# Kernel tuning notes

Hardware: AMD Instinct MI355X
Metric: run time of the kernel (lower is better)

The kernel has to match this reference:

```python
import jax, jax.numpy as jnp
import numpy as np

N = 100_000   # nodes
E = 1_600_000 # edges
G = 64        # graphs in batch
IN_FEAT, H = 8, 16
NUM_CLASSES = 4


def _glorot(key, fi, fo):
    lim = float(np.sqrt(6.0 / (fi + fo)))
    return jax.random.uniform(key, (fi, fo), jnp.float32, -lim, lim)


def setup_inputs() -> dict:
    key = jax.random.key(0)
    ks = jax.random.split(key, 12)
    inp = {
        "x": jax.random.normal(ks[0], (N, IN_FEAT), jnp.float32),
        "edge_src": jax.random.randint(ks[1], (E,), 0, N, dtype=jnp.int32),
        "edge_dst": jax.random.randint(ks[2], (E,), 0, N, dtype=jnp.int32),
        "batch": jnp.sort(jax.random.randint(ks[3], (N,), 0, G, dtype=jnp.int32)),
    }
    dims = [(IN_FEAT, H), (H, 2 * H), (2 * H, 4 * H), (4 * H, 8 * H)]
    for i, (fi, fo) in enumerate(dims, 1):
        inp[f"W{i}"] = _glorot(ks[3 + i], fi, fo)
        inp[f"b{i}"] = jnp.zeros((fo,), jnp.float32)
    # PReLU slopes (torch default init 0.25, single parameter)
    inp["a1"] = jnp.float32(0.25)
    inp["a2"] = jnp.float32(0.25)
    inp["a3"] = jnp.float32(0.25)
    inp["Wlin"] = _glorot(ks[8], 8 * H, NUM_CLASSES)
    inp["blin"] = jnp.zeros((NUM_CLASSES,), jnp.float32)
    return inp


def _prelu(x, a):
    return jnp.where(x >= 0, x, a * x)


def reference(x, edge_src, edge_dst, batch,
              W1, b1, W2, b2, W3, b3, W4, b4,
              a1, a2, a3, Wlin, blin):
    # GCNConv: add self-loops, symmetric normalization D^-1/2 A_hat D^-1/2
    loops = jnp.arange(N, dtype=edge_src.dtype)
    src = jnp.concatenate([edge_src, loops])  # [E+N]
    dst = jnp.concatenate([edge_dst, loops])
    deg = jax.ops.segment_sum(jnp.ones_like(src, jnp.float32), dst, num_segments=N)
    dinv = jax.lax.rsqrt(jnp.maximum(deg, 1.0))
    norm = dinv[src] * dinv[dst]  # [E+N]

    def gcn(h, W, b):
        h = h @ W                                   # [N, Fout]
        msg = h[src] * norm[:, None]                # gather + edge scale
        return jax.ops.segment_sum(msg, dst, num_segments=N) + b

    h = _prelu(gcn(x, W1, b1), a1)
    h = _prelu(gcn(h, W2, b2), a2)
    h = _prelu(gcn(h, W3, b3), a3)
    h = gcn(h, W4, b4)

    # global mean pool over graphs
    sums = jax.ops.segment_sum(h, batch, num_segments=G)          # [G, 8H]
    cnts = jax.ops.segment_sum(jnp.ones((N,), jnp.float32), batch, num_segments=G)
    pooled = sums / jnp.maximum(cnts, 1.0)[:, None]
    # dropout(p=0.25) is identity at inference
    return pooled @ Wlin + blin                                    # [G, 4]
```

## Files before the change

### kernel.cpp

```cpp
#include <hip/hip_runtime.h>
#include <hip/hip_fp16.h>

#define NN 100000
#define NE 1600000
#define NG 64

#define BSHIFT 7
#define BUCKW (1 << BSHIFT)
#define NBUCK ((NN + BUCKW - 1) >> BSHIFT)
#define BCAP 2560
#define BIN_CHUNK 4096

union H8 { float4 f4; __half2 h2[4]; };
union H4 { float2 f2; __half2 h2[2]; };
__device__ __forceinline__ void h8_to_f(const H8& h, float* f) {
    float2 a = __half22float2(h.h2[0]);
    float2 b = __half22float2(h.h2[1]);
    float2 c = __half22float2(h.h2[2]);
    float2 d = __half22float2(h.h2[3]);
    f[0]=a.x; f[1]=a.y; f[2]=b.x; f[3]=b.y; f[4]=c.x; f[5]=c.y; f[6]=d.x; f[7]=d.y;
}
__device__ __forceinline__ H8 f_to_h8(const float* f) {
    H8 h;
    h.h2[0] = __floats2half2_rn(f[0], f[1]);
    h.h2[1] = __floats2half2_rn(f[2], f[3]);
    h.h2[2] = __floats2half2_rn(f[4], f[5]);
    h.h2[3] = __floats2half2_rn(f[6], f[7]);
    return h;
}
__device__ __forceinline__ float prelu_f(float x, float s) {
    return fmaxf(x, 0.f) + s * fminf(x, 0.f);
}

__global__ __launch_bounds__(256) void bin_kernel(const int* __restrict__ src,
                                                  const int* __restrict__ dst,
                                                  int* __restrict__ bcnt,
                                                  unsigned* __restrict__ binned, int E) {
    __shared__ int h[NBUCK];
    __shared__ int cur[NBUCK];
    for (int i = threadIdx.x; i < NBUCK; i += 256) h[i] = 0;
    __syncthreads();
    int base = blockIdx.x * BIN_CHUNK;
    int end = base + BIN_CHUNK; if (end > E) end = E;
    for (int e = base + threadIdx.x; e < end; e += 256)
        atomicAdd(&h[dst[e] >> BSHIFT], 1);
    __syncthreads();
    for (int i = threadIdx.x; i < NBUCK; i += 256) {
        int c = h[i];
        cur[i] = c ? (i * BCAP + atomicAdd(&bcnt[i], c)) : 0;
    }
    __syncthreads();
    for (int e = base + threadIdx.x; e < end; e += 256) {
        unsigned s = (unsigned)src[e], d = (unsigned)dst[e];
        int pos = atomicAdd(&cur[d >> BSHIFT], 1);
        binned[pos] = (s << BSHIFT) | (d & (BUCKW - 1));
    }
}

__global__ __launch_bounds__(256) void build_csr_kernel(
    const unsigned* __restrict__ binned, const int* __restrict__ bucket_cnt,
    const float4* __restrict__ x4, float4* __restrict__ xs,
    int* __restrict__ deg, float* __restrict__ dinv,
    int* __restrict__ roff, int* __restrict__ csr_src, int n) {
    __shared__ int ldeg[BUCKW];
    __shared__ int lscan[2][BUCKW];
    __shared__ int lcur[BUCKW];
    int b = blockIdx.x;
    int tid = threadIdx.x;
    for (int i = tid; i < BUCKW; i += 256) ldeg[i] = 0;
    __syncthreads();
    int start = b * BCAP, cnt = bucket_cnt[b];
    for (int k = tid; k < cnt; k += 256)
        atomicAdd(&ldeg[binned[start + k] & (BUCKW - 1)], 1);
    __syncthreads();
    if (tid < BUCKW) lscan[0][tid] = ldeg[tid];
    __syncthreads();
    int cur = 0;
    for (int off = 1; off < BUCKW; off <<= 1) {
        int x = 0;
        if (tid < BUCKW) {
            x = lscan[cur][tid];
            if (tid >= off) x += lscan[cur][tid - off];
        }
        __syncthreads();
        if (tid < BUCKW) lscan[cur ^ 1][tid] = x;
        __syncthreads();
        cur ^= 1;
    }
    int v0 = b << BSHIFT;
    if (tid < BUCKW) {
        int v = v0 + tid;
        if (v < n) {
            int dg = ldeg[tid];
            deg[v] = dg;
            float dv = rsqrtf((float)dg + 1.0f);
            dinv[v] = dv;
            float4 h0 = x4[(size_t)v * 2 + 0];
            float4 h1 = x4[(size_t)v * 2 + 1];
            h0.x *= dv; h0.y *= dv; h0.z *= dv; h0.w *= dv;
            h1.x *= dv; h1.y *= dv; h1.z *= dv; h1.w *= dv;
            xs[(size_t)v * 2 + 0] = h0;
            xs[(size_t)v * 2 + 1] = h1;
            int r = start + lscan[cur][tid] - dg;
            roff[v] = r;
            lcur[tid] = r;
        }
    }
    __syncthreads();
    for (int k = tid; k < cnt; k += 256) {
        unsigned e = binned[start + k];
        int pos = atomicAdd(&lcur[e & (BUCKW - 1)], 1);
        csr_src[pos] = (int)(e >> BSHIFT);
    }
}

__global__ __launch_bounds__(256) void makeM_kernel(
    const float* __restrict__ W4, const float* __restrict__ b4,
    const float* __restrict__ Wlin, const float* __restrict__ blin,
    float* __restrict__ M, float* __restrict__ bb) {
    int t = threadIdx.x;
    int k = t >> 2, c = t & 3;
    float m = 0.f;
    for (int j = 0; j < 128; ++j) m += W4[k * 128 + j] * Wlin[j * 4 + c];
    M[k * 4 + c] = m;
    if (t < 4) {
        float v = blin[t];
        for (int j = 0; j < 128; ++j) v += b4[j] * Wlin[j * 4 + t];
        bb[t] = v;
    }
}

__global__ __launch_bounds__(256) void aggmm1_kernel(
    const float4* __restrict__ xs, const int* __restrict__ row_off,
    const int* __restrict__ deg, const float* __restrict__ dinv,
    const int* __restrict__ csr_src, const float* __restrict__ W1,
    const float* __restrict__ b1, const float* __restrict__ a1,
    float2* __restrict__ Aout2, int n) {
    __shared__ float Wl[8 * 16];
    for (int i = threadIdx.x; i < 8 * 16; i += 256) Wl[i] = W1[i];
    __syncthreads();
    int idx = blockIdx.x * 256 + threadIdx.x;
    if (idx >= n * 4) return;
    int v = idx >> 2;
    int c = idx & 1;
    int h = (idx >> 1) & 1;
    float4 acc = (h == 0) ? xs[(size_t)v * 2 + c] : make_float4(0.f, 0.f, 0.f, 0.f);
    int start = row_off[v], cnt = deg[v];
    int mid = cnt >> 1;
    int beg = h ? mid : 0;
    int myend = h ? cnt : mid;
    const int* __restrict__ row = csr_src + start;
    int j = beg;
    for (; j + 4 <= myend; j += 4) {
        int s0 = row[j], s1 = row[j + 1], s2 = row[j + 2], s3 = row[j + 3];
        float4 a0 = xs[(size_t)s0 * 2 + c];
        float4 a1v = xs[(size_t)s1 * 2 + c];
        float4 a2 = xs[(size_t)s2 * 2 + c];
        float4 a3 = xs[(size_t)s3 * 2 + c];
        acc.x += (a0.x + a1v.x) + (a2.x + a3.x);
        acc.y += (a0.y + a1v.y) + (a2.y + a3.y);
        acc.z += (a0.z + a1v.z) + (a2.z + a3.z);
        acc.w += (a0.w + a1v.w) + (a2.w + a3.w);
    }
    for (; j < myend; ++j) {
        int s = row[j];
        float4 a = xs[(size_t)s * 2 + c];
        acc.x += a.x; acc.y += a.y; acc.z += a.z; acc.w += a.w;
    }
    acc.x += __shfl_xor(acc.x, 2, 64);
    acc.y += __shfl_xor(acc.y, 2, 64);
    acc.z += __shfl_xor(acc.z, 2, 64);
    acc.w += __shfl_xor(acc.w, 2, 64);
    float dvv = dinv[v];
    float t[4] = { acc.x * dvv, acc.y * dvv, acc.z * dvv, acc.w * dvv };
    float po[4];
#pragma unroll
    for (int k = 0; k < 4; ++k) po[k] = __shfl_xor(t[k], 1, 64);
    int ow = (h * 2 + c) * 4;
    int e0 = c * 4, e1 = 4 - e0;
    float accm[4];
#pragma unroll
    for (int q = 0; q < 4; ++q) accm[q] = b1[ow + q];
#pragma unroll
    for (int k = 0; k < 4; ++k) {
        float r1 = t[k], r2 = po[k];
        const float* w1 = &Wl[(e0 + k) * 16 + ow];
        const float* w2 = &Wl[(e1 + k) * 16 + ow];
#pragma unroll
        for (int q = 0; q < 4; ++q) accm[q] += r1 * w1[q] + r2 * w2[q];
    }
    float s = *a1;
    float o[4];
#pragma unroll
    for (int q = 0; q < 4; ++q) o[q] = prelu_f(accm[q], s) * dvv;
    H4 ho;
    ho.h2[0] = __floats2half2_rn(o[0], o[1]);
    ho.h2[1] = __floats2half2_rn(o[2], o[3]);
    Aout2[(size_t)v * 4 + (h * 2 + c)] = ho.f2;
}

__global__ __launch_bounds__(256) void aggmm2_kernel(
    const float4* __restrict__ hs, const int* __restrict__ row_off,
    const int* __restrict__ deg, const float* __restrict__ dinv,
    const int* __restrict__ csr_src, const float* __restrict__ W2,
    const float* __restrict__ b2, const float* __restrict__ a2,
    float4* __restrict__ Aout, int n) {
    __shared__ float Wl[16 * 32];
    for (int i = threadIdx.x; i < 16 * 32; i += 256) Wl[i] = W2[i];
    __syncthreads();
    int idx = blockIdx.x * 256 + threadIdx.x;
    if (idx >= n * 4) return;
    int v = idx >> 2;
    int c = idx & 1;
    int h = (idx >> 1) & 1;
    float a[8];
    if (h == 0) { H8 t; t.f4 = hs[(size_t)v * 2 + c]; h8_to_f(t, a); }
    else {
#pragma unroll
        for (int k = 0; k < 8; ++k) a[k] = 0.f;
    }
    int start = row_off[v], cnt = deg[v];
    int mid = cnt >> 1;
    int beg = h ? mid : 0;
    int myend = h ? cnt : mid;
    const int* __restrict__ row = csr_src + start;
    int j = beg;
    for (; j + 4 <= myend; j += 4) {
        H8 hh[4];
#pragma unroll
        for (int q = 0; q < 4; ++q) hh[q].f4 = hs[(size_t)row[j + q] * 2 + c];
#pragma unroll
        for (int q = 0; q < 4; ++q) {
            float f[8]; h8_to_f(hh[q], f);
#pragma unroll
            for (int k = 0; k < 8; ++k) a[k] += f[k];
        }
    }
    for (; j < myend; ++j) {
        H8 t; t.f4 = hs[(size_t)row[j] * 2 + c];
        float f[8]; h8_to_f(t, f);
#pragma unroll
        for (int k = 0; k < 8; ++k) a[k] += f[k];
    }
#pragma unroll
    for (int k = 0; k < 8; ++k) a[k] += __shfl_xor(a[k], 2, 64);
    float dvv = dinv[v];
#pragma unroll
    for (int k = 0; k < 8; ++k) a[k] *= dvv;
    float pa[8];
#pragma unroll
    for (int k = 0; k < 8; ++k) pa[k] = __shfl_xor(a[k], 1, 64);
    int ow = (h * 2 + c) * 8;
    int e0 = c * 8, e1 = 8 - e0;
    float accm[8];
#pragma unroll
    for (int q = 0; q < 8; ++q) accm[q] = b2[ow + q];
#pragma unroll
    for (int k = 0; k < 8; ++k) {
        float r1 = a[k], r2 = pa[k];
        const float* w1 = &Wl[(e0 + k) * 32 + ow];
        const float* w2 = &Wl[(e1 + k) * 32 + ow];
#pragma unroll
        for (int q = 0; q < 8; ++q) accm[q] += r1 * w1[q] + r2 * w2[q];
    }
    float s = *a2;
    float o[8];
#pragma unroll
    for (int q = 0; q < 8; ++q) o[q] = prelu_f(accm[q], s) * dvv;
    H8 ho = f_to_h8(o);
    Aout[(size_t)v * 4 + (h * 2 + c)] = ho.f4;
}

__global__ __launch_bounds__(256) void aggmm3_kernel(
    const float4* __restrict__ hs, const int* __restrict__ row_off,
    const int* __restrict__ deg, const float* __restrict__ dinv,
    const int* __restrict__ csr_src, const float* __restrict__ W3,
    const float* __restrict__ b3, const float* __restrict__ a3,
    const float* __restrict__ M, float4* __restrict__ z, int n) {
    __shared__ float Wl[32 * 64];
    __shared__ float Ml[64 * 4];
    for (int i = threadIdx.x; i < 32 * 64; i += 256) Wl[i] = W3[i];
    for (int i = threadIdx.x; i < 64 * 4; i += 256) Ml[i] = M[i];
    __syncthreads();
    int idx = blockIdx.x * 256 + threadIdx.x;
    if (idx >= n * 8) return;
    int v = idx >> 3;
    int c = idx & 3;
    int h = (idx >> 2) & 1;
    float a[8];
    if (h == 0) { H8 t; t.f4 = hs[(size_t)v * 4 + c]; h8_to_f(t, a); }
    else {
#pragma unroll
        for (int k = 0; k < 8; ++k) a[k] = 0.f;
    }
    int start = row_off[v], cnt = deg[v];
    int mid = cnt >> 1;
    int beg = h ? mid : 0;
    int myend = h ? cnt : mid;
    const int* __restrict__ row = csr_src + start;
    int j = beg;
    for (; j + 4 <= myend; j += 4) {
        H8 hh[4];
#pragma unroll
        for (int q = 0; q < 4; ++q) hh[q].f4 = hs[(size_t)row[j + q] * 4 + c];
#pragma unroll
        for (int q = 0; q < 4; ++q) {
            float f[8]; h8_to_f(hh[q], f);
#pragma unroll
            for (int k = 0; k < 8; ++k) a[k] += f[k];
        }
    }
    for (; j < myend; ++j) {
        H8 t; t.f4 = hs[(size_t)row[j] * 4 + c];
        float f[8]; h8_to_f(t, f);
#pragma unroll
        for (int k = 0; k < 8; ++k) a[k] += f[k];
    }
#pragma unroll
    for (int k = 0; k < 8; ++k) a[k] += __shfl_xor(a[k], 4, 64);
    float dvv = dinv[v];
#pragma unroll
    for (int k = 0; k < 8; ++k) a[k] *= dvv;
    int ow = (h * 4 + c) * 8;
    float accm[8];
#pragma unroll
    for (int q = 0; q < 8; ++q) accm[q] = b3[ow + q];
#pragma unroll
    for (int m = 0; m < 4; ++m) {
        float cur[8];
        if (m == 0) {
#pragma unroll
            for (int k = 0; k < 8; ++k) cur[k] = a[k];
        } else {
#pragma unroll
            for (int k = 0; k < 8; ++k) cur[k] = __shfl_xor(a[k], m, 64);
        }
        int eb = (c ^ m) * 8;
#pragma unroll
        for (int k = 0; k < 8; ++k) {
            float rk = cur[k];
            const float* wp = &Wl[(eb + k) * 64 + ow];
#pragma unroll
            for (int q = 0; q < 8; ++q) accm[q] += rk * wp[q];
        }
    }
    float s = *a3;
    float px = 0.f, py = 0.f, pz = 0.f, pw = 0.f;
#pragma unroll
    for (int q = 0; q < 8; ++q) {
        float o = prelu_f(accm[q], s) * dvv;
        const float* mp = &Ml[(ow + q) * 4];
        px += o * mp[0]; py += o * mp[1]; pz += o * mp[2]; pw += o * mp[3];
    }
#pragma unroll
    for (int mask = 1; mask <= 4; mask <<= 1) {
        px += __shfl_xor(px, mask, 64);
        py += __shfl_xor(py, mask, 64);
        pz += __shfl_xor(pz, mask, 64);
        pw += __shfl_xor(pw, mask, 64);
    }
    if ((idx & 7) == 0) z[v] = make_float4(px, py, pz, pw);
}

__global__ __launch_bounds__(256) void aggpool4_kernel(
    const float4* __restrict__ z, const int* __restrict__ row_off,
    const int* __restrict__ deg, const float* __restrict__ dinv,
    const int* __restrict__ csr_src, const int* __restrict__ batch,
    float* __restrict__ sums, float* __restrict__ cnt, int n) {
    __shared__ float lacc[NG * 4];
    __shared__ float lcnt[NG];
    int tid = threadIdx.x;
    if (tid < NG * 4) lacc[tid] = 0.f;
    if (tid < NG) lcnt[tid] = 0.f;
    __syncthreads();
    int idx = blockIdx.x * 256 + tid;
    bool valid = (idx < n * 2);
    int v = idx >> 1;
    int h = idx & 1;
    float cx = 0.f, cy = 0.f, cz = 0.f, cw = 0.f, rc = 0.f;
    int g = -1;
    if (valid) {
        float4 acc = (h == 0) ? z[v] : make_float4(0.f, 0.f, 0.f, 0.f);
        int start = row_off[v], dcnt = deg[v];
        int mid = dcnt >> 1;
        int beg = h ? mid : 0;
        int myend = h ? dcnt : mid;
        const int* __restrict__ row = csr_src + start;
        int j = beg;
        for (; j + 4 <= myend; j += 4) {
            float4 a0 = z[row[j]];
            float4 a1 = z[row[j + 1]];
            float4 a2 = z[row[j + 2]];
            float4 a3 = z[row[j + 3]];
            acc.x += (a0.x + a1.x) + (a2.x + a3.x);
            acc.y += (a0.y + a1.y) + (a2.y + a3.y);
            acc.z += (a0.z + a1.z) + (a2.z + a3.z);
            acc.w += (a0.w + a1.w) + (a2.w + a3.w);
        }
        for (; j < myend; ++j) {
            float4 a = z[row[j]];
            acc.x += a.x; acc.y += a.y; acc.z += a.z; acc.w += a.w;
        }
        cx = acc.x; cy = acc.y; cz = acc.z; cw = acc.w;
        g = batch[v];
    }
    cx += __shfl_xor(cx, 1, 64);
    cy += __shfl_xor(cy, 1, 64);
    cz += __shfl_xor(cz, 1, 64);
    cw += __shfl_xor(cw, 1, 64);
    if (valid) {
        float dv = dinv[v];
        cx *= dv; cy *= dv; cz *= dv; cw *= dv;
    }
    if (!valid || h == 1) { cx = cy = cz = cw = 0.f; rc = 0.f; }
    else rc = 1.f;
    int g0 = __shfl(g, 0, 64);
    if (__all(g == g0 || !valid)) {
#pragma unroll
        for (int mask = 32; mask >= 1; mask >>= 1) {
            cx += __shfl_xor(cx, mask, 64);
            cy += __shfl_xor(cy, mask, 64);
            cz += __shfl_xor(cz, mask, 64);
            cw += __shfl_xor(cw, mask, 64);
            rc += __shfl_xor(rc, mask, 64);
        }
        if ((tid & 63) == 0 && g0 >= 0) {
            float* lp = &lacc[g0 * 4];
            atomicAdd(lp + 0, cx); atomicAdd(lp + 1, cy);
            atomicAdd(lp + 2, cz); atomicAdd(lp + 3, cw);
            atomicAdd(&lcnt[g0], rc);
        }
    } else if (valid && h == 0) {
        float* lp = &lacc[g * 4];
        atomicAdd(lp + 0, cx); atomicAdd(lp + 1, cy);
        atomicAdd(lp + 2, cz); atomicAdd(lp + 3, cw);
        atomicAdd(&lcnt[g], 1.f);
    }
    __syncthreads();
    if (tid < NG * 4) {
        float val = lacc[tid];
        if (val != 0.f) atomicAdd(&sums[tid], val);
    }
    if (tid < NG) {
        float val = lcnt[tid];
        if (val != 0.f) atomicAdd(&cnt[tid], val);
    }
}

__global__ void head_kernel(const float* __restrict__ sums, const float* __restrict__ cnt,
                            const float* __restrict__ bb, float* __restrict__ out) {
    int t = threadIdx.x;
    int g = t >> 2, c = t & 3;
    out[t] = sums[t] / fmaxf(cnt[g], 1.f) + bb[c];
}

extern "C" void kernel_launch(void* const* d_in, const int* in_sizes, int n_in,
                              void* d_out, int out_size, void* d_ws, size_t ws_size,
                              hipStream_t stream) {
    const float* x    = (const float*)d_in[0];
    const int* esrc   = (const int*)d_in[1];
    const int* edst   = (const int*)d_in[2];
    const int* batch  = (const int*)d_in[3];
    const float* W1 = (const float*)d_in[4],  *b1 = (const float*)d_in[5];
    const float* W2 = (const float*)d_in[6],  *b2 = (const float*)d_in[7];
    const float* W3 = (const float*)d_in[8],  *b3 = (const float*)d_in[9];
    const float* W4 = (const float*)d_in[10], *b4 = (const float*)d_in[11];
    const float* a1 = (const float*)d_in[12];
    const float* a2 = (const float*)d_in[13];
    const float* a3 = (const float*)d_in[14];
    const float* Wlin = (const float*)d_in[15], *blin = (const float*)d_in[16];
    float* out = (float*)d_out;

    const int N = NN, E = NE;
    const int NBIN = (E + BIN_CHUNK - 1) / BIN_CHUNK;

    char* w = (char*)d_ws;
    size_t off = 0;
    auto alloc = [&](size_t bytes) { size_t r = off; off += (bytes + 255) & ~(size_t)255; return r; };
    size_t o_bcnt = alloc((size_t)NBUCK * 4);
    size_t o_pool = alloc((size_t)NG * 4 * 4);
    size_t o_cnt  = alloc((size_t)NG * 4);
    size_t zero_bytes = off;
    size_t o_deg  = alloc((size_t)N * 4);
    size_t o_dinv = alloc((size_t)N * 4);
    size_t o_roff = alloc((size_t)N * 4);
    size_t o_xs   = alloc((size_t)N * 8 * 4);
    size_t o_csrc = alloc((size_t)NBUCK * BCAP * 4);
    size_t o_bin  = alloc((size_t)NBUCK * BCAP * 4);
    size_t o_A1   = alloc((size_t)N * 16 * 2);
    size_t o_A2   = alloc((size_t)N * 32 * 2);
    size_t o_z    = alloc((size_t)N * 4 * 4);
    size_t o_M    = alloc((size_t)64 * 4 * 4);
    size_t o_bb   = alloc((size_t)4 * 4);
    (void)ws_size;
    int*      bcnt   = (int*)(w + o_bcnt);
    float*    pool   = (float*)(w + o_pool);
    float*    cnt    = (float*)(w + o_cnt);
    int*      deg    = (int*)(w + o_deg);
    float*    dinv   = (float*)(w + o_dinv);
    int*      roff   = (int*)(w + o_roff);
    float4*   xs     = (float4*)(w + o_xs);
    int*      csrc   = (int*)(w + o_csrc);
    unsigned* binned = (unsigned*)(w + o_bin);
    float2*   A1_2   = (float2*)(w + o_A1);
    float4*   A1     = (float4*)(w + o_A1);
    float4*   A2     = (float4*)(w + o_A2);
    float4*   z      = (float4*)(w + o_z);
    float*    M      = (float*)(w + o_M);
    float*    bb     = (float*)(w + o_bb);

    hipMemsetAsync(w, 0, zero_bytes, stream);

    makeM_kernel<<<1, 256, 0, stream>>>(W4, b4, Wlin, blin, M, bb);

    bin_kernel<<<NBIN, 256, 0, stream>>>(esrc, edst, bcnt, binned, E);
    build_csr_kernel<<<NBUCK, 256, 0, stream>>>(binned, bcnt, (const float4*)x, xs,
                                                deg, dinv, roff, csrc, N);

    aggmm1_kernel<<<(N * 4 + 255) / 256, 256, 0, stream>>>(
        xs, roff, deg, dinv, csrc, W1, b1, a1, A1_2, N);

    aggmm2_kernel<<<(N * 4 + 255) / 256, 256, 0, stream>>>(
        A1, roff, deg, dinv, csrc, W2, b2, a2, A2, N);

    aggmm3_kernel<<<(N * 8 + 255) / 256, 256, 0, stream>>>(
        A2, roff, deg, dinv, csrc, W3, b3, a3, M, z, N);

    aggpool4_kernel<<<(N * 2 + 255) / 256, 256, 0, stream>>>(
        z, roff, deg, dinv, csrc, batch, pool, cnt, N);
    head_kernel<<<1, 256, 0, stream>>>(pool, cnt, bb, out);
}
```

Baseline: 224.6 us.

## Use coarser 1024-node buckets for CSR build with register-cached edge binning

The buckets used to bin edges by destination grow from 128 to 1024 nodes, giving 98 buckets instead of 782. The CSR build kernel now runs one 1024-thread block per bucket. The binning kernel loads each edge's src and dst into registers once and reuses them for both the histogram and scatter passes, with smaller chunks per block. This cuts global atomics on bucket counters and repeated edge reads. In exchange, far fewer blocks run the CSR build, each does a longer 10-step scan, and the bucket capacity bound (18432) must hold for the random inputs.

```diff
diff --git a/kernel.cpp b/kernel.cpp
--- a/kernel.cpp
+++ b/kernel.cpp
@@ -5,11 +5,11 @@
 #define NE 1600000
 #define NG 64
 
-#define BSHIFT 7
-#define BUCKW (1 << BSHIFT)
-#define NBUCK ((NN + BUCKW - 1) >> BSHIFT)
-#define BCAP 2560
-#define BIN_CHUNK 4096
+#define BSHIFT_C 10
+#define BUCKW_C (1 << BSHIFT_C)
+#define NBUCK_C ((NN + BUCKW_C - 1) >> BSHIFT_C)
+#define BCAP_C 18432
+#define BIN_CHUNK 2048
 
 union H8 { float4 f4; __half2 h2[4]; };
 union H4 { float2 f2; __half2 h2[2]; };
@@ -36,81 +36,89 @@
                                                   const int* __restrict__ dst,
                                                   int* __restrict__ bcnt,
                                                   unsigned* __restrict__ binned, int E) {
-    __shared__ int h[NBUCK];
-    __shared__ int cur[NBUCK];
-    for (int i = threadIdx.x; i < NBUCK; i += 256) h[i] = 0;
+    __shared__ int h[NBUCK_C];
+    __shared__ int cur[NBUCK_C];
+    int tid = threadIdx.x;
+    for (int i = tid; i < NBUCK_C; i += 256) h[i] = 0;
     __syncthreads();
     int base = blockIdx.x * BIN_CHUNK;
     int end = base + BIN_CHUNK; if (end > E) end = E;
-    for (int e = base + threadIdx.x; e < end; e += 256)
-        atomicAdd(&h[dst[e] >> BSHIFT], 1);
-    __syncthreads();
-    for (int i = threadIdx.x; i < NBUCK; i += 256) {
+    int ms[8], md[8];
+#pragma unroll
+    for (int k = 0; k < 8; ++k) {
+        int e = base + k * 256 + tid;
+        if (e < end) { ms[k] = src[e]; md[k] = dst[e]; }
+    }
+#pragma unroll
+    for (int k = 0; k < 8; ++k) {
+        int e = base + k * 256 + tid;
+        if (e < end) atomicAdd(&h[md[k] >> BSHIFT_C], 1);
+    }
+    __syncthreads();
+    for (int i = tid; i < NBUCK_C; i += 256) {
         int c = h[i];
-        cur[i] = c ? (i * BCAP + atomicAdd(&bcnt[i], c)) : 0;
-    }
-    __syncthreads();
-    for (int e = base + threadIdx.x; e < end; e += 256) {
-        unsigned s = (unsigned)src[e], d = (unsigned)dst[e];
-        int pos = atomicAdd(&cur[d >> BSHIFT], 1);
-        binned[pos] = (s << BSHIFT) | (d & (BUCKW - 1));
-    }
-}
-
-__global__ __launch_bounds__(256) void build_csr_kernel(
+        cur[i] = c ? (i * BCAP_C + atomicAdd(&bcnt[i], c)) : 0;
+    }
+    __syncthreads();
+#pragma unroll
+    for (int k = 0; k < 8; ++k) {
+        int e = base + k * 256 + tid;
+        if (e < end) {
+            unsigned s = (unsigned)ms[k], d = (unsigned)md[k];
+            int pos = atomicAdd(&cur[d >> BSHIFT_C], 1);
+            binned[pos] = (s << BSHIFT_C) | (d & (BUCKW_C - 1));
+        }
+    }
+}
+
+__global__ __launch_bounds__(1024) void build_csr_kernel(
     const unsigned* __restrict__ binned, const int* __restrict__ bucket_cnt,
     const float4* __restrict__ x4, float4* __restrict__ xs,
     int* __restrict__ deg, float* __restrict__ dinv,
     int* __restrict__ roff, int* __restrict__ csr_src, int n) {
-    __shared__ int ldeg[BUCKW];
-    __shared__ int lscan[2][BUCKW];
-    __shared__ int lcur[BUCKW];
-    int b = blockIdx.x;
+    __shared__ int ldeg[BUCKW_C];
+    __shared__ int lscan[2][BUCKW_C];
+    __shared__ int lcur[BUCKW_C];
+    int cb = blockIdx.x;
     int tid = threadIdx.x;
-    for (int i = tid; i < BUCKW; i += 256) ldeg[i] = 0;
-    __syncthreads();
-    int start = b * BCAP, cnt = bucket_cnt[b];
-    for (int k = tid; k < cnt; k += 256)
-        atomicAdd(&ldeg[binned[start + k] & (BUCKW - 1)], 1);
-    __syncthreads();
-    if (tid < BUCKW) lscan[0][tid] = ldeg[tid];
+    ldeg[tid] = 0;
+    __syncthreads();
+    int start = cb * BCAP_C, cnt = bucket_cnt[cb];
+    for (int k = tid; k < cnt; k += 1024)
+        atomicAdd(&ldeg[binned[start + k] & (BUCKW_C - 1)], 1);
+    __syncthreads();
+    lscan[0][tid] = ldeg[tid];
     __syncthreads();
     int cur = 0;
-    for (int off = 1; off < BUCKW; off <<= 1) {
-        int x = 0;
-        if (tid < BUCKW) {
-            x = lscan[cur][tid];
-            if (tid >= off) x += lscan[cur][tid - off];
-        }
+    for (int off = 1; off < BUCKW_C; off <<= 1) {
+        int x = lscan[cur][tid];
+        if (tid >= off) x += lscan[cur][tid - off];
         __syncthreads();
-        if (tid < BUCKW) lscan[cur ^ 1][tid] = x;
+        lscan[cur ^ 1][tid] = x;
         __syncthreads();
         cur ^= 1;
     }
-    int v0 = b << BSHIFT;
-    if (tid < BUCKW) {
-        int v = v0 + tid;
-        if (v < n) {
-            int dg = ldeg[tid];
-            deg[v] = dg;
-            float dv = rsqrtf((float)dg + 1.0f);
-            dinv[v] = dv;
-            float4 h0 = x4[(size_t)v * 2 + 0];
-            float4 h1 = x4[(size_t)v * 2 + 1];
-            h0.x *= dv; h0.y *= dv; h0.z *= dv; h0.w *= dv;
-            h1.x *= dv; h1.y *= dv; h1.z *= dv; h1.w *= dv;
-            xs[(size_t)v * 2 + 0] = h0;
-            xs[(size_t)v * 2 + 1] = h1;
-            int r = start + lscan[cur][tid] - dg;
-            roff[v] = r;
-            lcur[tid] = r;
-        }
-    }
-    __syncthreads();
-    for (int k = tid; k < cnt; k += 256) {
+    int v = (cb << BSHIFT_C) + tid;
+    if (v < n) {
+        int dg = ldeg[tid];
+        deg[v] = dg;
+        float dv = rsqrtf((float)dg + 1.0f);
+        dinv[v] = dv;
+        float4 h0 = x4[(size_t)v * 2 + 0];
+        float4 h1 = x4[(size_t)v * 2 + 1];
+        h0.x *= dv; h0.y *= dv; h0.z *= dv; h0.w *= dv;
+        h1.x *= dv; h1.y *= dv; h1.z *= dv; h1.w *= dv;
+        xs[(size_t)v * 2 + 0] = h0;
+        xs[(size_t)v * 2 + 1] = h1;
+        int r = start + lscan[cur][tid] - dg;
+        roff[v] = r;
+        lcur[tid] = r;
+    }
+    __syncthreads();
+    for (int k = tid; k < cnt; k += 1024) {
         unsigned e = binned[start + k];
-        int pos = atomicAdd(&lcur[e & (BUCKW - 1)], 1);
-        csr_src[pos] = (int)(e >> BSHIFT);
+        int pos = atomicAdd(&lcur[e & (BUCKW_C - 1)], 1);
+        csr_src[pos] = (int)(e >> BSHIFT_C);
     }
 }
 
@@ -477,7 +485,7 @@
     char* w = (char*)d_ws;
     size_t off = 0;
     auto alloc = [&](size_t bytes) { size_t r = off; off += (bytes + 255) & ~(size_t)255; return r; };
-    size_t o_bcnt = alloc((size_t)NBUCK * 4);
+    size_t o_bcnt = alloc((size_t)NBUCK_C * 4);
     size_t o_pool = alloc((size_t)NG * 4 * 4);
     size_t o_cnt  = alloc((size_t)NG * 4);
     size_t zero_bytes = off;
@@ -485,8 +493,8 @@
     size_t o_dinv = alloc((size_t)N * 4);
     size_t o_roff = alloc((size_t)N * 4);
     size_t o_xs   = alloc((size_t)N * 8 * 4);
-    size_t o_csrc = alloc((size_t)NBUCK * BCAP * 4);
-    size_t o_bin  = alloc((size_t)NBUCK * BCAP * 4);
+    size_t o_csrc = alloc((size_t)NBUCK_C * BCAP_C * 4);
+    size_t o_bin  = alloc((size_t)NBUCK_C * BCAP_C * 4);
     size_t o_A1   = alloc((size_t)N * 16 * 2);
     size_t o_A2   = alloc((size_t)N * 32 * 2);
     size_t o_z    = alloc((size_t)N * 4 * 4);
@@ -514,8 +522,8 @@
     makeM_kernel<<<1, 256, 0, stream>>>(W4, b4, Wlin, blin, M, bb);
 
     bin_kernel<<<NBIN, 256, 0, stream>>>(esrc, edst, bcnt, binned, E);
-    build_csr_kernel<<<NBUCK, 256, 0, stream>>>(binned, bcnt, (const float4*)x, xs,
-                                                deg, dinv, roff, csrc, N);
+    build_csr_kernel<<<NBUCK_C, 1024, 0, stream>>>(binned, bcnt, (const float4*)x, xs,
+                                                   deg, dinv, roff, csrc, N);
 
     aggmm1_kernel<<<(N * 4 + 255) / 256, 256, 0, stream>>>(
         xs, roff, deg, dinv, csrc, W1, b1, a1, A1_2, N);
```

Result: no change. 228.2 us (+1.6%).
